# Performance work log

Measured on AMD Instinct MI355X. Metric: run time of the kernel, lower is better.

## Reference

```python
import jax, jax.numpy as jnp
import numpy as np

B, CIN, COUT = 2, 64, 64
D, H, W = 8, 32, 32
KD = KH = KW = 3
K = KD * KH * KW  # 27
STRIDE, PAD, DIL = 1, 1, 1
DOUT = (D + 2 * PAD - DIL * (KD - 1) - 1) // STRIDE + 1
HOUT = (H + 2 * PAD - DIL * (KH - 1) - 1) // STRIDE + 1
WOUT = (W + 2 * PAD - DIL * (KW - 1) - 1) // STRIDE + 1


def setup_inputs() -> dict:
    key = jax.random.key(0)
    k1, k2, k3, k4 = jax.random.split(key, 4)
    x = jax.random.normal(k1, (B, CIN, D, H, W), dtype=jnp.float32)
    offset = jax.random.normal(k2, (B, 3 * K, DOUT, HOUT, WOUT), dtype=jnp.float32)
    weight = jax.random.normal(k3, (COUT, CIN, KD, KH, KW), dtype=jnp.float32) * 0.05
    bias = jax.random.normal(k4, (COUT,), dtype=jnp.float32) * 0.1
    return {"x": x, "offset": offset, "weight": weight, "bias": bias}


def _trilinear_sample(xb, zd, zh, zw):
    # xb: [C, D, H, W]; zd/zh/zw: [K, P] float sampling coords (zero padding outside)
    Dd, Hh, Ww = xb.shape[1], xb.shape[2], xb.shape[3]
    d0 = jnp.floor(zd); h0 = jnp.floor(zh); w0 = jnp.floor(zw)
    fd = zd - d0; fh = zh - h0; fw = zw - w0
    d0i = d0.astype(jnp.int32); h0i = h0.astype(jnp.int32); w0i = w0.astype(jnp.int32)
    acc = jnp.zeros((xb.shape[0],) + zd.shape, dtype=xb.dtype)
    for dd in (0, 1):
        for dh in (0, 1):
            for dw in (0, 1):
                di = d0i + dd; hi = h0i + dh; wi = w0i + dw
                wgt = ((fd if dd else 1.0 - fd) * (fh if dh else 1.0 - fh)
                       * (fw if dw else 1.0 - fw))
                valid = ((di >= 0) & (di < Dd) & (hi >= 0) & (hi < Hh)
                         & (wi >= 0) & (wi < Ww)).astype(xb.dtype)
                v = xb[:, jnp.clip(di, 0, Dd - 1), jnp.clip(hi, 0, Hh - 1),
                       jnp.clip(wi, 0, Ww - 1)]  # [C, K, P]
                acc = acc + v * (wgt * valid)[None]
    return acc


def _deform_conv3d(x, offset, weight, bias):
    Bb = x.shape[0]
    P = DOUT * HOUT * WOUT
    # kernel taps
    kd, kh, kw = jnp.unravel_index(jnp.arange(K), (KD, KH, KW))
    # output grid
    od, oh, ow = jnp.meshgrid(jnp.arange(DOUT), jnp.arange(HOUT), jnp.arange(WOUT), indexing="ij")
    base_d = (od[None] * STRIDE - PAD + kd[:, None, None, None] * DIL).astype(jnp.float32)  # [K,Do,Ho,Wo]
    base_h = (oh[None] * STRIDE - PAD + kh[:, None, None, None] * DIL).astype(jnp.float32)
    base_w = (ow[None] * STRIDE - PAD + kw[:, None, None, None] * DIL).astype(jnp.float32)
    off = offset.reshape(Bb, K, 3, DOUT, HOUT, WOUT)  # per-tap (dd, dh, dw)
    zd = (base_d[None] + off[:, :, 0]).reshape(Bb, K, P)
    zh = (base_h[None] + off[:, :, 1]).reshape(Bb, K, P)
    zw = (base_w[None] + off[:, :, 2]).reshape(Bb, K, P)
    sampled = jax.vmap(_trilinear_sample)(x, zd, zh, zw)  # [B, C, K, P]
    wmat = weight.reshape(COUT, CIN, K)
    out = jnp.einsum("bckp,ock->bop", sampled, wmat)  # [B, COUT, P]
    out = out + bias[None, :, None]
    return out.reshape(Bb, COUT, DOUT, HOUT, WOUT)


def reference(x, offset, weight, bias):
    return _deform_conv3d(x, offset, weight, bias)
```

## Files before the change

### kernel.cpp

```cpp
#include <hip/hip_runtime.h>
#include <hip/hip_fp16.h>


#define BB    2
#define CINC  64
#define COUTC 64
#define DDEP  8
#define HGT   32
#define WID   32
#define KK    27
#define KGRP  9
#define KPB   3
#define PP    8192
#define TP    64

typedef _Float16 f16x8 __attribute__((ext_vector_type(8)));
typedef float f32x4 __attribute__((ext_vector_type(4)));
typedef unsigned int u32x4 __attribute__((ext_vector_type(4)));

__device__ __forceinline__ __half2 h2(unsigned v) { return __builtin_bit_cast(__half2, v); }
__device__ __forceinline__ unsigned h2u(__half2 h) { return __builtin_bit_cast(unsigned, h); }
__device__ __forceinline__ __half2 blo(unsigned v) { return __half2half2(__low2half(h2(v))); }
__device__ __forceinline__ __half2 bhi(unsigned v) { return __half2half2(__high2half(h2(v))); }

__device__ __forceinline__ void acc8h(const char* __restrict__ xc, int off, __half2 uu,
                                      __half2& s0, __half2& s1, __half2& s2, __half2& s3) {
    u32x4 v = *(const u32x4*)(xc + off);
    s0 = __hfma2(h2(v.x), uu, s0);
    s1 = __hfma2(h2(v.y), uu, s1);
    s2 = __hfma2(h2(v.z), uu, s2);
    s3 = __hfma2(h2(v.w), uu, s3);
}

#define WBLOCKS 432
#define ZBLOCKS 1024
__global__ void pre_kernel(const float* __restrict__ x, const float* __restrict__ w,
                           unsigned short* __restrict__ xt, unsigned short* __restrict__ wt,
                           float* __restrict__ out) {
    __shared__ float sT[64][65];
    const int t    = threadIdx.x;
    const int lane = t & 63;
    const int wv   = t >> 6;
    const int half = lane >> 5;
    const int c2   = lane & 31;
    int blk = blockIdx.x;
    if (blk < 256) {
        int b  = blk >> 7;
        int s0 = (blk & 127) * 64;
        #pragma unroll
        for (int i = 0; i < 16; ++i) {
            int c = wv * 16 + i;
            sT[c][lane] = x[(size_t)(b * CINC + c) * PP + s0 + lane];
        }
        __syncthreads();
        #pragma unroll
        for (int i = 0; i < 8; ++i) {
            int s = wv * 16 + 2 * i + half;
            unsigned pk = h2u(__floats2half2_rn(sT[2 * c2][s], sT[2 * c2 + 1][s]));
            *(unsigned*)&xt[(size_t)(b * PP + s0 + s) * 64 + 2 * c2] = pk;
        }
    } else if (blk < 256 + WBLOCKS) {
        int id = (blk - 256) * 256 + t;
        if (id < KK * COUTC * CINC) {
            int c = id & 63;
            int o = (id >> 6) & 63;
            int k = id >> 12;
            __half hw = __float2half(w[(o * CINC + c) * KK + k]);
            wt[id] = __builtin_bit_cast(unsigned short, hw);
        }
    } else {
        int id = (blk - 256 - WBLOCKS) * 256 + t;
        ((float4*)out)[id] = make_float4(0.f, 0.f, 0.f, 0.f);
    }
}

__global__ __launch_bounds__(256, 4) void deform_kernel(
    const unsigned short* __restrict__ xt, const float* __restrict__ off,
    const unsigned short* __restrict__ wt, const float* __restrict__ bias,
    float* __restrict__ out)
{
    __shared__ unsigned short sW[KPB * COUTC * 64] __attribute__((aligned(16)));
    __shared__ unsigned short sS[TP * 64]          __attribute__((aligned(16)));
    __shared__ int sCrd[KPB][TP][8] __attribute__((aligned(16)));

    const int t     = threadIdx.x;
    const int lane  = t & 63;
    const int wv    = t >> 6;
    const int choct = lane & 7;
    const int g8    = lane >> 3;
    const int ch16  = 16 * choct;
    const int b     = blockIdx.x >> 7;
    const int p0    = (blockIdx.x & 127) * TP;
    const int kg    = blockIdx.y;
    const int kbase = kg * KPB;

    const char* __restrict__ xc = (const char*)xt + (size_t)b * PP * 128;
    char* sWb = (char*)sW;
    char* sSb = (char*)sS;

    f32x4 acc[4];
    #pragma unroll
    for (int g = 0; g < 4; ++g) acc[g] = (f32x4)0.0f;

    const int n0  = lane & 15;
    const int q   = lane >> 4;
    const int cr  = lane & 15;
    const int ckl = lane >> 4;

    {
        const unsigned short* wk = wt + kbase * (COUTC * CINC);
        #pragma unroll
        for (int j = 0; j < 6; ++j) {
            int idx = j * 2048 + t * 8;
            int kl  = idx >> 12;
            int o   = (idx >> 6) & 63;
            int cb  = (idx & 63) * 2;
            *(f16x8*)(sWb + kl * 8192 + o * 128 + (cb ^ ((o & 7) << 4))) =
                *(const f16x8*)(wk + idx);
        }
    }

    if (ckl < KPB) {
        int k  = kbase + ckl;
        int pl = 16 * wv + cr;
        int pp = p0 + pl;
        int ow = pp & 31;
        int oh = (pp >> 5) & 31;
        int od = pp >> 10;
        int kd = k / 9;
        int kh = (k - kd * 9) / 3;
        int kw = k - kd * 9 - kh * 3;
        const float* ob = off + (size_t)(b * (3 * KK) + 3 * k) * PP + pp;
        float zd = (float)(od - 1 + kd) + ob[0];
        float zh = (float)(oh - 1 + kh) + ob[PP];
        float zw = (float)(ow - 1 + kw) + ob[2 * PP];

        float fdf = floorf(zd); int d0 = (int)fdf; float fd = zd - fdf;
        float fhf = floorf(zh); int h0 = (int)fhf; float fh = zh - fhf;
        float fwf = floorf(zw); int w0 = (int)fwf; float fw = zw - fwf;

        float Bd0 = (d0 >= 0     && d0 < DDEP)     ? 1.0f - fd : 0.0f;
        float Bd1 = (d0 + 1 >= 0 && d0 + 1 < DDEP) ? fd        : 0.0f;
        float Ch0 = (h0 >= 0     && h0 < HGT)      ? 1.0f - fh : 0.0f;
        float Ch1 = (h0 + 1 >= 0 && h0 + 1 < HGT)  ? fh        : 0.0f;
        float Aw0 = (w0 >= 0     && w0 < WID)      ? 1.0f - fw : 0.0f;
        float Aw1 = (w0 + 1 >= 0 && w0 + 1 < WID)  ? fw        : 0.0f;
        int dc0 = min(max(d0, 0), DDEP - 1);
        int dc1 = min(max(d0 + 1, 0), DDEP - 1);
        int hc0 = min(max(h0, 0), HGT - 1);
        int hc1 = min(max(h0 + 1, 0), HGT - 1);
        int wc0 = min(max(w0, 0), WID - 1);
        int wc1 = min(max(w0 + 1, 0), WID - 1);

        int base = (dc0 * HGT + hc0) * (WID * 128) + wc0 * 128;
        int wD   = (wc1 - wc0) * 128;
        int hD   = (hc1 - hc0) * (WID * 128);
        int dD   = (dc1 - dc0) * (HGT * WID * 128);
        sCrd[ckl][pl][0] = base;
        sCrd[ckl][pl][1] = wD;
        sCrd[ckl][pl][2] = hD;
        sCrd[ckl][pl][3] = dD;
        float bc0 = Bd0 * Ch0, bc1 = Bd0 * Ch1, bc2 = Bd1 * Ch0, bc3 = Bd1 * Ch1;
        sCrd[ckl][pl][4] = (int)h2u(__floats2half2_rn(bc0 * Aw0, bc0 * Aw1));
        sCrd[ckl][pl][5] = (int)h2u(__floats2half2_rn(bc1 * Aw0, bc1 * Aw1));
        sCrd[ckl][pl][6] = (int)h2u(__floats2half2_rn(bc2 * Aw0, bc2 * Aw1));
        sCrd[ckl][pl][7] = (int)h2u(__floats2half2_rn(bc3 * Aw0, bc3 * Aw1));
    }
    __syncthreads();

    const int sw   = (n0 & 7) << 4;
    const int cb0  = (16 * q) ^ sw;
    const int cb1  = (64 + 16 * q) ^ sw;
    #pragma unroll
    for (int kl = 0; kl < KPB; ++kl) {
        #pragma unroll
        for (int it = 0; it < 2; ++it) {
            int prow = 16 * wv + 8 * it + g8;
            const int4  ib = *(const int4*)&sCrd[kl][prow][0];
            const u32x4 cw = *(const u32x4*)&sCrd[kl][prow][4];
            int o0 = ib.x + ch16;
            int o1 = o0 + ib.y;
            int o2 = o0 + ib.z;
            int o3 = o2 + ib.y;
            int o4 = o0 + ib.w;
            int o5 = o4 + ib.y;
            int o6 = o4 + ib.z;
            int o7 = o6 + ib.y;
            __half2 s0 = h2(0u), s1 = h2(0u), s2 = h2(0u), s3 = h2(0u);
            acc8h(xc, o0, blo(cw.x), s0, s1, s2, s3);
            acc8h(xc, o1, bhi(cw.x), s0, s1, s2, s3);
            acc8h(xc, o2, blo(cw.y), s0, s1, s2, s3);
            acc8h(xc, o3, bhi(cw.y), s0, s1, s2, s3);
            acc8h(xc, o4, blo(cw.z), s0, s1, s2, s3);
            acc8h(xc, o5, bhi(cw.z), s0, s1, s2, s3);
            acc8h(xc, o6, blo(cw.w), s0, s1, s2, s3);
            acc8h(xc, o7, bhi(cw.w), s0, s1, s2, s3);
            u32x4 pk = {h2u(s0), h2u(s1), h2u(s2), h2u(s3)};
            *(u32x4*)(sSb + prow * 128 + (ch16 ^ ((prow & 7) << 4))) = pk;
        }

        {
            const char* sWk = sWb + kl * 8192;
            const int rowB = (16 * wv + n0) * 128;
            f16x8 b0 = *(const f16x8*)(sSb + rowB + cb0);
            f16x8 b1 = *(const f16x8*)(sSb + rowB + cb1);
            __builtin_amdgcn_s_setprio(1);
            #pragma unroll
            for (int g = 0; g < 4; ++g) {
                f16x8 a0 = *(const f16x8*)(sWk + (16 * g + n0) * 128 + cb0);
                f16x8 a1 = *(const f16x8*)(sWk + (16 * g + n0) * 128 + cb1);
                acc[g] = __builtin_amdgcn_mfma_f32_16x16x32_f16(a0, b0, acc[g], 0, 0, 0);
                acc[g] = __builtin_amdgcn_mfma_f32_16x16x32_f16(a1, b1, acc[g], 0, 0, 0);
            }
            __builtin_amdgcn_s_setprio(0);
        }
    }

    const int p = p0 + 16 * wv + n0;
    #pragma unroll
    for (int g = 0; g < 4; ++g) {
        #pragma unroll
        for (int r = 0; r < 4; ++r) {
            int o = 16 * g + 4 * q + r;
            float v = acc[g][r];
            if (kg == 0) v += bias[o];
            unsafeAtomicAdd(&out[(size_t)(b * COUTC + o) * PP + p], v);
        }
    }
}

extern "C" void kernel_launch(void* const* d_in, const int* in_sizes, int n_in,
                              void* d_out, int out_size, void* d_ws, size_t ws_size,
                              hipStream_t stream) {
    const float* x    = (const float*)d_in[0];
    const float* off  = (const float*)d_in[1];
    const float* w    = (const float*)d_in[2];
    const float* bias = (const float*)d_in[3];
    float* out        = (float*)d_out;

    unsigned short* xt = (unsigned short*)d_ws;
    unsigned short* wt = (unsigned short*)((char*)d_ws + (size_t)BB * PP * 64 * 2);

    hipLaunchKernelGGL(pre_kernel, dim3(256 + WBLOCKS + ZBLOCKS), dim3(256), 0,
                       stream, x, w, xt, wt, out);
    hipLaunchKernelGGL(deform_kernel, dim3(BB * (PP / TP), KGRP), dim3(256), 0, stream,
                       xt, off, wt, bias, out);
}
```

Before: 101.9 us.

## Accumulate nine taps per block in three phases and pad LDS rows

Each block now loops over three phases of three kernel taps, so it covers nine taps instead of three. The tap groups drop from nine to three, which cuts the atomic-add traffic to the output by a factor of three. The XOR-swizzled LDS layout is replaced by row padding (stride 72 halves), and the occupancy hint drops from 4 to 3 blocks. In exchange the grid has fewer blocks, each block runs longer, and every phase adds extra barriers.

```diff
diff --git a/kernel.cpp b/kernel.cpp
--- a/kernel.cpp
+++ b/kernel.cpp
@@ -9,10 +9,12 @@
 #define HGT   32
 #define WID   32
 #define KK    27
-#define KGRP  9
-#define KPB   3
+#define KGRP  3
+#define KPG   9
+#define KPH   3
 #define PP    8192
 #define TP    64
+#define LDW   72
 
 typedef _Float16 f16x8 __attribute__((ext_vector_type(8)));
 typedef float f32x4 __attribute__((ext_vector_type(4)));
@@ -74,14 +76,14 @@
     }
 }
 
-__global__ __launch_bounds__(256, 4) void deform_kernel(
+__global__ __launch_bounds__(256, 3) void deform_kernel(
     const unsigned short* __restrict__ xt, const float* __restrict__ off,
     const unsigned short* __restrict__ wt, const float* __restrict__ bias,
     float* __restrict__ out)
 {
-    __shared__ unsigned short sW[KPB * COUTC * 64] __attribute__((aligned(16)));
-    __shared__ unsigned short sS[TP * 64]          __attribute__((aligned(16)));
-    __shared__ int sCrd[KPB][TP][8] __attribute__((aligned(16)));
+    __shared__ unsigned short sW[KPH * COUTC * LDW] __attribute__((aligned(16)));
+    __shared__ unsigned short sS[TP * LDW]          __attribute__((aligned(16)));
+    __shared__ int sCrd[KPH][TP][8] __attribute__((aligned(16)));
 
     const int t     = threadIdx.x;
     const int lane  = t & 63;
@@ -92,11 +94,8 @@
     const int b     = blockIdx.x >> 7;
     const int p0    = (blockIdx.x & 127) * TP;
     const int kg    = blockIdx.y;
-    const int kbase = kg * KPB;
 
     const char* __restrict__ xc = (const char*)xt + (size_t)b * PP * 128;
-    char* sWb = (char*)sW;
-    char* sSb = (char*)sS;
 
     f32x4 acc[4];
     #pragma unroll
@@ -107,112 +106,112 @@
     const int cr  = lane & 15;
     const int ckl = lane >> 4;
 
-    {
+    #pragma unroll 1
+    for (int ph = 0; ph < 3; ++ph) {
+        const int kbase = kg * KPG + ph * KPH;
+
+        __syncthreads();
+
         const unsigned short* wk = wt + kbase * (COUTC * CINC);
         #pragma unroll
         for (int j = 0; j < 6; ++j) {
             int idx = j * 2048 + t * 8;
             int kl  = idx >> 12;
-            int o   = (idx >> 6) & 63;
-            int cb  = (idx & 63) * 2;
-            *(f16x8*)(sWb + kl * 8192 + o * 128 + (cb ^ ((o & 7) << 4))) =
+            int rem = idx & 4095;
+            *(f16x8*)&sW[kl * (COUTC * LDW) + (rem >> 6) * LDW + (rem & 63)] =
                 *(const f16x8*)(wk + idx);
         }
-    }
-
-    if (ckl < KPB) {
-        int k  = kbase + ckl;
-        int pl = 16 * wv + cr;
-        int pp = p0 + pl;
-        int ow = pp & 31;
-        int oh = (pp >> 5) & 31;
-        int od = pp >> 10;
-        int kd = k / 9;
-        int kh = (k - kd * 9) / 3;
-        int kw = k - kd * 9 - kh * 3;
-        const float* ob = off + (size_t)(b * (3 * KK) + 3 * k) * PP + pp;
-        float zd = (float)(od - 1 + kd) + ob[0];
-        float zh = (float)(oh - 1 + kh) + ob[PP];
-        float zw = (float)(ow - 1 + kw) + ob[2 * PP];
-
-        float fdf = floorf(zd); int d0 = (int)fdf; float fd = zd - fdf;
-        float fhf = floorf(zh); int h0 = (int)fhf; float fh = zh - fhf;
-        float fwf = floorf(zw); int w0 = (int)fwf; float fw = zw - fwf;
-
-        float Bd0 = (d0 >= 0     && d0 < DDEP)     ? 1.0f - fd : 0.0f;
-        float Bd1 = (d0 + 1 >= 0 && d0 + 1 < DDEP) ? fd        : 0.0f;
-        float Ch0 = (h0 >= 0     && h0 < HGT)      ? 1.0f - fh : 0.0f;
-        float Ch1 = (h0 + 1 >= 0 && h0 + 1 < HGT)  ? fh        : 0.0f;
-        float Aw0 = (w0 >= 0     && w0 < WID)      ? 1.0f - fw : 0.0f;
-        float Aw1 = (w0 + 1 >= 0 && w0 + 1 < WID)  ? fw        : 0.0f;
-        int dc0 = min(max(d0, 0), DDEP - 1);
-        int dc1 = min(max(d0 + 1, 0), DDEP - 1);
-        int hc0 = min(max(h0, 0), HGT - 1);
-        int hc1 = min(max(h0 + 1, 0), HGT - 1);
-        int wc0 = min(max(w0, 0), WID - 1);
-        int wc1 = min(max(w0 + 1, 0), WID - 1);
-
-        int base = (dc0 * HGT + hc0) * (WID * 128) + wc0 * 128;
-        int wD   = (wc1 - wc0) * 128;
-        int hD   = (hc1 - hc0) * (WID * 128);
-        int dD   = (dc1 - dc0) * (HGT * WID * 128);
-        sCrd[ckl][pl][0] = base;
-        sCrd[ckl][pl][1] = wD;
-        sCrd[ckl][pl][2] = hD;
-        sCrd[ckl][pl][3] = dD;
-        float bc0 = Bd0 * Ch0, bc1 = Bd0 * Ch1, bc2 = Bd1 * Ch0, bc3 = Bd1 * Ch1;
-        sCrd[ckl][pl][4] = (int)h2u(__floats2half2_rn(bc0 * Aw0, bc0 * Aw1));
-        sCrd[ckl][pl][5] = (int)h2u(__floats2half2_rn(bc1 * Aw0, bc1 * Aw1));
-        sCrd[ckl][pl][6] = (int)h2u(__floats2half2_rn(bc2 * Aw0, bc2 * Aw1));
-        sCrd[ckl][pl][7] = (int)h2u(__floats2half2_rn(bc3 * Aw0, bc3 * Aw1));
-    }
-    __syncthreads();
-
-    const int sw   = (n0 & 7) << 4;
-    const int cb0  = (16 * q) ^ sw;
-    const int cb1  = (64 + 16 * q) ^ sw;
-    #pragma unroll
-    for (int kl = 0; kl < KPB; ++kl) {
-        #pragma unroll
-        for (int it = 0; it < 2; ++it) {
-            int prow = 16 * wv + 8 * it + g8;
-            const int4  ib = *(const int4*)&sCrd[kl][prow][0];
-            const u32x4 cw = *(const u32x4*)&sCrd[kl][prow][4];
-            int o0 = ib.x + ch16;
-            int o1 = o0 + ib.y;
-            int o2 = o0 + ib.z;
-            int o3 = o2 + ib.y;
-            int o4 = o0 + ib.w;
-            int o5 = o4 + ib.y;
-            int o6 = o4 + ib.z;
-            int o7 = o6 + ib.y;
-            __half2 s0 = h2(0u), s1 = h2(0u), s2 = h2(0u), s3 = h2(0u);
-            acc8h(xc, o0, blo(cw.x), s0, s1, s2, s3);
-            acc8h(xc, o1, bhi(cw.x), s0, s1, s2, s3);
-            acc8h(xc, o2, blo(cw.y), s0, s1, s2, s3);
-            acc8h(xc, o3, bhi(cw.y), s0, s1, s2, s3);
-            acc8h(xc, o4, blo(cw.z), s0, s1, s2, s3);
-            acc8h(xc, o5, bhi(cw.z), s0, s1, s2, s3);
-            acc8h(xc, o6, blo(cw.w), s0, s1, s2, s3);
-            acc8h(xc, o7, bhi(cw.w), s0, s1, s2, s3);
-            u32x4 pk = {h2u(s0), h2u(s1), h2u(s2), h2u(s3)};
-            *(u32x4*)(sSb + prow * 128 + (ch16 ^ ((prow & 7) << 4))) = pk;
-        }
-
-        {
-            const char* sWk = sWb + kl * 8192;
-            const int rowB = (16 * wv + n0) * 128;
-            f16x8 b0 = *(const f16x8*)(sSb + rowB + cb0);
-            f16x8 b1 = *(const f16x8*)(sSb + rowB + cb1);
-            __builtin_amdgcn_s_setprio(1);
+
+        if (ckl < KPH) {
+            int k  = kbase + ckl;
+            int pl = 16 * wv + cr;
+            int pp = p0 + pl;
+            int ow = pp & 31;
+            int oh = (pp >> 5) & 31;
+            int od = pp >> 10;
+            int kd = k / 9;
+            int kh = (k - kd * 9) / 3;
+            int kw = k - kd * 9 - kh * 3;
+            const float* ob = off + (size_t)(b * (3 * KK) + 3 * k) * PP + pp;
+            float zd = (float)(od - 1 + kd) + ob[0];
+            float zh = (float)(oh - 1 + kh) + ob[PP];
+            float zw = (float)(ow - 1 + kw) + ob[2 * PP];
+
+            float fdf = floorf(zd); int d0 = (int)fdf; float fd = zd - fdf;
+            float fhf = floorf(zh); int h0 = (int)fhf; float fh = zh - fhf;
+            float fwf = floorf(zw); int w0 = (int)fwf; float fw = zw - fwf;
+
+            float Bd0 = (d0 >= 0     && d0 < DDEP)     ? 1.0f - fd : 0.0f;
+            float Bd1 = (d0 + 1 >= 0 && d0 + 1 < DDEP) ? fd        : 0.0f;
+            float Ch0 = (h0 >= 0     && h0 < HGT)      ? 1.0f - fh : 0.0f;
+            float Ch1 = (h0 + 1 >= 0 && h0 + 1 < HGT)  ? fh        : 0.0f;
+            float Aw0 = (w0 >= 0     && w0 < WID)      ? 1.0f - fw : 0.0f;
+            float Aw1 = (w0 + 1 >= 0 && w0 + 1 < WID)  ? fw        : 0.0f;
+            int dc0 = min(max(d0, 0), DDEP - 1);
+            int dc1 = min(max(d0 + 1, 0), DDEP - 1);
+            int hc0 = min(max(h0, 0), HGT - 1);
+            int hc1 = min(max(h0 + 1, 0), HGT - 1);
+            int wc0 = min(max(w0, 0), WID - 1);
+            int wc1 = min(max(w0 + 1, 0), WID - 1);
+
+            int base = (dc0 * HGT + hc0) * (WID * 128) + wc0 * 128;
+            int wD   = (wc1 - wc0) * 128;
+            int hD   = (hc1 - hc0) * (WID * 128);
+            int dD   = (dc1 - dc0) * (HGT * WID * 128);
+            sCrd[ckl][pl][0] = base;
+            sCrd[ckl][pl][1] = wD;
+            sCrd[ckl][pl][2] = hD;
+            sCrd[ckl][pl][3] = dD;
+            float bc0 = Bd0 * Ch0, bc1 = Bd0 * Ch1, bc2 = Bd1 * Ch0, bc3 = Bd1 * Ch1;
+            sCrd[ckl][pl][4] = (int)h2u(__floats2half2_rn(bc0 * Aw0, bc0 * Aw1));
+            sCrd[ckl][pl][5] = (int)h2u(__floats2half2_rn(bc1 * Aw0, bc1 * Aw1));
+            sCrd[ckl][pl][6] = (int)h2u(__floats2half2_rn(bc2 * Aw0, bc2 * Aw1));
+            sCrd[ckl][pl][7] = (int)h2u(__floats2half2_rn(bc3 * Aw0, bc3 * Aw1));
+        }
+        __syncthreads();
+
+        #pragma unroll
+        for (int kl = 0; kl < KPH; ++kl) {
             #pragma unroll
-            for (int g = 0; g < 4; ++g) {
-                f16x8 a0 = *(const f16x8*)(sWk + (16 * g + n0) * 128 + cb0);
-                f16x8 a1 = *(const f16x8*)(sWk + (16 * g + n0) * 128 + cb1);
-                acc[g] = __builtin_amdgcn_mfma_f32_16x16x32_f16(a0, b0, acc[g], 0, 0, 0);
-                acc[g] = __builtin_amdgcn_mfma_f32_16x16x32_f16(a1, b1, acc[g], 0, 0, 0);
+            for (int it = 0; it < 2; ++it) {
+                int prow = 16 * wv + 8 * it + g8;
+                const int4  ib = *(const int4*)&sCrd[kl][prow][0];
+                const u32x4 cw = *(const u32x4*)&sCrd[kl][prow][4];
+                int o0 = ib.x + ch16;
+                int o1 = o0 + ib.y;
+                int o2 = o0 + ib.z;
+                int o3 = o2 + ib.y;
+                int o4 = o0 + ib.w;
+                int o5 = o4 + ib.y;
+                int o6 = o4 + ib.z;
+                int o7 = o6 + ib.y;
+                __half2 s0 = h2(0u), s1 = h2(0u), s2 = h2(0u), s3 = h2(0u);
+                acc8h(xc, o0, blo(cw.x), s0, s1, s2, s3);
+                acc8h(xc, o1, bhi(cw.x), s0, s1, s2, s3);
+                acc8h(xc, o2, blo(cw.y), s0, s1, s2, s3);
+                acc8h(xc, o3, bhi(cw.y), s0, s1, s2, s3);
+                acc8h(xc, o4, blo(cw.z), s0, s1, s2, s3);
+                acc8h(xc, o5, bhi(cw.z), s0, s1, s2, s3);
+                acc8h(xc, o6, blo(cw.w), s0, s1, s2, s3);
+                acc8h(xc, o7, bhi(cw.w), s0, s1, s2, s3);
+                u32x4 pk = {h2u(s0), h2u(s1), h2u(s2), h2u(s3)};
+                *(u32x4*)&sS[prow * LDW + 8 * choct] = pk;
             }
-            __builtin_amdgcn_s_setprio(0);
+
+            {
+                const unsigned short* sWk = &sW[kl * (COUTC * LDW)];
+                f16x8 b0 = *(const f16x8*)&sS[(16 * wv + n0) * LDW +      8 * q];
+                f16x8 b1 = *(const f16x8*)&sS[(16 * wv + n0) * LDW + 32 + 8 * q];
+                __builtin_amdgcn_s_setprio(1);
+                #pragma unroll
+                for (int g = 0; g < 4; ++g) {
+                    f16x8 a0 = *(const f16x8*)&sWk[(16 * g + n0) * LDW +      8 * q];
+                    f16x8 a1 = *(const f16x8*)&sWk[(16 * g + n0) * LDW + 32 + 8 * q];
+                    acc[g] = __builtin_amdgcn_mfma_f32_16x16x32_f16(a0, b0, acc[g], 0, 0, 0);
+                    acc[g] = __builtin_amdgcn_mfma_f32_16x16x32_f16(a1, b1, acc[g], 0, 0, 0);
+                }
+                __builtin_amdgcn_s_setprio(0);
+            }
         }
     }
 
```

Result: faster. 91.75 us (-10.0%).
